# Optimization experiments

Hardware: AMD Instinct MI355X
Metric: run time of the kernel (lower is better)

## Reference

```python
import jax, jax.numpy as jnp
import numpy as np

HEADS = 16
D_MODEL = 1024
D_HEAD = D_MODEL // HEADS


def setup_inputs() -> dict:
    key = jax.random.key(0)
    ks = jax.random.split(key, 12)
    B, S = 4, 2048
    scale = D_MODEL ** -0.5
    inp = {
        "q": jax.random.normal(ks[0], (B, S, D_MODEL), jnp.float32),
        "k": jax.random.normal(ks[1], (B, S, D_MODEL), jnp.float32),
        "v": jax.random.normal(ks[2], (B, S, D_MODEL), jnp.float32),
        # causal mask: True = masked position
        "mask": jnp.triu(jnp.ones((S, S), bool), k=1)[None].repeat(B, axis=0),
        "wq": jax.random.normal(ks[3], (D_MODEL, D_MODEL), jnp.float32) * scale,
        "bq": jnp.zeros((D_MODEL,), jnp.float32),
        "wk": jax.random.normal(ks[4], (D_MODEL, D_MODEL), jnp.float32) * scale,
        "bk": jnp.zeros((D_MODEL,), jnp.float32),
        "wv": jax.random.normal(ks[5], (D_MODEL, D_MODEL), jnp.float32) * scale,
        "bv": jnp.zeros((D_MODEL,), jnp.float32),
        "wo": jax.random.normal(ks[6], (D_MODEL, D_MODEL), jnp.float32) * scale,
        "bo": jnp.zeros((D_MODEL,), jnp.float32),
    }
    return inp


def _split_head(x):
    B, S, _ = x.shape
    return x.reshape(B, S, HEADS, D_HEAD).transpose(0, 2, 1, 3)  # [B,H,S,D]


def reference(q, k, v, mask, wq, bq, wk, bk, wv, bv, wo, bo):
    # linear projections (torch Linear: x @ W^T + b)
    qh = _split_head(q @ wq.T + bq) * (D_HEAD ** -0.5)
    kh = _split_head(k @ wk.T + bk)
    vh = _split_head(v @ wv.T + bv)
    # scores [B,H,Sq,Sk]
    scores = jnp.einsum("bhqd,bhkd->bhqk", qh, kh)
    scores = jnp.where(mask[:, None, :, :], -1e20, scores)
    weights = jax.nn.softmax(scores, axis=-1)  # dropout p=0 in eval
    ctx = jnp.einsum("bhqk,bhkd->bhqd", weights, vh)
    B, H, S, D = ctx.shape
    ctx = ctx.transpose(0, 2, 1, 3).reshape(B, S, H * D)
    return ctx @ wo.T + bo
```

## Files before the change

### kernel.cpp

```cpp
#include <hip/hip_runtime.h>
#include <hip/hip_bf16.h>
#include <cstdint>
#include <cstddef>

typedef unsigned short u16;
typedef unsigned int u32;
using short8  = __attribute__((ext_vector_type(8))) short;
using f32x4   = __attribute__((ext_vector_type(4))) float;
using f32x16  = __attribute__((ext_vector_type(16))) float;
using u32x4   = __attribute__((ext_vector_type(4))) u32;

#define SCALE_Q 0.18033688011112043f

#define WAITVM(N) asm volatile("s_waitcnt vmcnt(" #N ")" ::: "memory")

__device__ inline u16 f2bf(float f) {
  return __builtin_bit_cast(u16, __float2bfloat16(f));
}

__device__ inline u32 cvt_pk_bf16(float a, float b) {
  u32 r;
  asm("v_cvt_pk_bf16_f32 %0, %1, %2" : "=v"(r) : "v"(a), "v"(b));
  return r;
}

__device__ inline f32x4 mfma16(short8 a, short8 b, f32x4 c) {
  return __builtin_amdgcn_mfma_f32_16x16x32_bf16(a, b, c, 0, 0, 0);
}
__device__ inline f32x16 mfma32(short8 a, short8 b, f32x16 c) {
  return __builtin_amdgcn_mfma_f32_32x32x16_bf16(a, b, c, 0, 0, 0);
}

__device__ inline void gload16(const void* g, void* l) {
  __builtin_amdgcn_global_load_lds(
      (const __attribute__((address_space(1))) void*)g,
      (__attribute__((address_space(3))) void*)l,
      16, 0, 0);
}

__global__ __launch_bounds__(256)
void prep(const float* __restrict__ q, const float* __restrict__ k,
          const float* __restrict__ v,
          const float* __restrict__ wq, const float* __restrict__ wk,
          const float* __restrict__ wv, const float* __restrict__ wo,
          u16* __restrict__ Wb, u16* __restrict__ Act) {
  const int c = blockIdx.x * 256 + threadIdx.x;
  const float* src;
  u16* dst;
  float sc = 1.f;
  size_t off;
  if (c < 524288) {
    const int m = c >> 17;
    off = (size_t)(c & 131071) * 8;
    src = (m == 0) ? wq : (m == 1) ? wk : (m == 2) ? wv : wo;
    if (m == 0) sc = SCALE_Q;
    dst = Wb + (size_t)m * 1048576;
  } else {
    const int c2 = c - 524288;
    const int m = c2 >> 20;
    off = (size_t)(c2 & 1048575) * 8;
    src = (m == 0) ? q : (m == 1) ? k : v;
    dst = Act + (size_t)m * 8388608;
  }
  f32x4 a = *(const f32x4*)(src + off);
  f32x4 b = *(const f32x4*)(src + off + 4);
  short8 vv;
#pragma unroll
  for (int j = 0; j < 4; ++j) { vv[j] = (short)f2bf(a[j] * sc); vv[4 + j] = (short)f2bf(b[j] * sc); }
  *(short8*)&dst[off] = vv;
}

struct GemmArgs {
  const u16* Act; const u16* ctx; const u16* Wb;
  const float* bq; const float* bk; const float* bv; const float* bo;
  u16* Qs; u16* Ks; u16* Vs; float* out;
};

__global__ __launch_bounds__(512)
void gemm_proj(GemmArgs ga, int modeBase) {
  const int mode = modeBase + blockIdx.z;
  const int bm = blockIdx.x, bn = blockIdx.y;
  const int tid = threadIdx.x;
  const int w = tid >> 6, lane = tid & 63;
  const int wr = w >> 1, wc = w & 1;
  const int l15 = lane & 15, g = lane >> 4;

  const u16* Am = (mode == 3) ? ga.ctx : ga.Act + (size_t)mode * 8388608;
  const u16* Wm = ga.Wb + (size_t)mode * 1048576;
  const float* bias = (mode == 0) ? ga.bq : (mode == 1) ? ga.bk : (mode == 2) ? ga.bv : ga.bo;

  __shared__ u16 As[4][256 * 32];
  __shared__ u16 Bs[4][128 * 32];

  f32x4 acc[4][4] = {};
  const int m0 = bm * 256, n0 = bn * 128;

  const int trow = tid >> 2;
  const int scol = (tid & 3) ^ ((tid >> 3) & 3);
  const int dstA0 = w * 512;
  const int dstA1 = 4096 + w * 512;
  const int dstB  = w * 512;

  auto stage = [&](int k0, int slot) {
    gload16(Am + (size_t)(m0 + trow) * 1024 + k0 + scol * 8,        &As[slot][dstA0]);
    gload16(Am + (size_t)(m0 + 128 + trow) * 1024 + k0 + scol * 8,  &As[slot][dstA1]);
    gload16(Wm + (size_t)(n0 + trow) * 1024 + k0 + scol * 8,        &Bs[slot][dstB]);
  };

  const int rsw = ((l15 >> 1) & 3);

  auto compute = [&](int slot) {
    short8 av[4], bv4[4];
#pragma unroll
    for (int mi = 0; mi < 4; ++mi)
      av[mi] = *(const short8*)&As[slot][(wr * 64 + mi * 16 + l15) * 32 + (g ^ rsw) * 8];
#pragma unroll
    for (int ni = 0; ni < 4; ++ni)
      bv4[ni] = *(const short8*)&Bs[slot][(wc * 64 + ni * 16 + l15) * 32 + (g ^ rsw) * 8];
#pragma unroll
    for (int mi = 0; mi < 4; ++mi)
#pragma unroll
      for (int ni = 0; ni < 4; ++ni)
        acc[mi][ni] = mfma16(av[mi], bv4[ni], acc[mi][ni]);
  };

  stage(0, 0);
  stage(32, 1);

  for (int tt = 0; tt < 28; tt += 4) {
#pragma unroll
    for (int u = 0; u < 4; ++u) {
      stage((tt + u + 2) * 32, (u + 2) & 3);
      __builtin_amdgcn_sched_barrier(0);
      WAITVM(6);
      __builtin_amdgcn_s_barrier();
      __builtin_amdgcn_sched_barrier(0);
      compute(u);
    }
  }
  stage(30 * 32, 2);
  __builtin_amdgcn_sched_barrier(0);
  WAITVM(6);
  __builtin_amdgcn_s_barrier();
  __builtin_amdgcn_sched_barrier(0);
  compute(0);

  stage(31 * 32, 3);
  __builtin_amdgcn_sched_barrier(0);
  WAITVM(6);
  __builtin_amdgcn_s_barrier();
  __builtin_amdgcn_sched_barrier(0);
  compute(1);

  WAITVM(3);
  __builtin_amdgcn_s_barrier();
  __builtin_amdgcn_sched_barrier(0);
  compute(2);

  WAITVM(0);
  __builtin_amdgcn_s_barrier();
  __builtin_amdgcn_sched_barrier(0);
  compute(3);

  float bvals[4];
#pragma unroll
  for (int ni = 0; ni < 4; ++ni)
    bvals[ni] = bias[n0 + wc * 64 + ni * 16 + l15] * ((mode == 0) ? SCALE_Q : 1.f);

  if (mode == 3) {
#pragma unroll
    for (int mi = 0; mi < 4; ++mi)
#pragma unroll
      for (int ni = 0; ni < 4; ++ni)
#pragma unroll
        for (int r = 0; r < 4; ++r) {
          const int m = m0 + wr * 64 + mi * 16 + g * 4 + r;
          const int n = n0 + wc * 64 + ni * 16 + l15;
          ga.out[(size_t)m * 1024 + n] = acc[mi][ni][r] + bvals[ni];
        }
  } else {
    u16* O = (mode == 0) ? ga.Qs : (mode == 1) ? ga.Ks : ga.Vs;
#pragma unroll
    for (int mi = 0; mi < 4; ++mi)
#pragma unroll
      for (int ni = 0; ni < 4; ++ni)
#pragma unroll
        for (int r = 0; r < 4; ++r) {
          const int m = m0 + wr * 64 + mi * 16 + g * 4 + r;
          const int n = n0 + wc * 64 + ni * 16 + l15;
          const int b = m >> 11, s = m & 2047, hh = n >> 6, d = n & 63;
          const float val = acc[mi][ni][r] + bvals[ni];
          const size_t base = (size_t)(b * 16 + hh) * 131072;
          size_t idx;
          if (mode == 2) {
            const int sp = (s & ~12) | ((s & 4) << 1) | ((s & 8) >> 1);
            const int kt = sp >> 5, w5 = sp & 31;
            const int j = ((d >> 5) << 1) | (w5 >> 4);
            const int hi2 = (w5 >> 3) & 1, e = w5 & 7;
            idx = base + (size_t)kt * 2048 + j * 512 + hi2 * 256 + (d & 31) * 8 + e;
          } else {
            const int s32 = s >> 5, l31 = s & 31;
            const int t2 = d >> 4, hi2 = (d >> 3) & 1, e = d & 7;
            idx = base + (size_t)s32 * 2048 + t2 * 512 + hi2 * 256 + l31 * 8 + e;
          }
          O[idx] = f2bf(val);
        }
  }
}

__global__ __launch_bounds__(256)
void attn_fwd(const u16* __restrict__ Qs, const u16* __restrict__ Ks,
              const u16* __restrict__ Vs, u16* __restrict__ ctx) {
  const int bh = blockIdx.x;
  const int qt = 15 - blockIdx.y;
  const int tid = threadIdx.x;
  const int w = tid >> 6, lane = tid & 63;
  const int l31 = lane & 31, hi = lane >> 5;

  const u16* Qb = Qs + (size_t)bh * 131072;
  const u16* Kb = Ks + (size_t)bh * 131072 + lane * 8;
  const u16* Vb = Vs + (size_t)bh * 131072 + lane * 8;
  const int b = bh >> 4, hh = bh & 15;

  const int qw0 = qt * 128 + w * 32;
  const int nkt = (qw0 >> 5) + 1;
  const int qrow = qw0 + l31;

  short8 qf[4];
  {
    const u16* qp = Qb + (size_t)(qw0 >> 5) * 2048 + lane * 8;
#pragma unroll
    for (int t = 0; t < 4; ++t) qf[t] = *(const short8*)(qp + t * 512);
  }

  f32x16 oacc0 = {}, oacc1 = {};
  float lsum = 0.f;

  auto body = [&](const short8* kf, const short8* vf, int kt, bool last) {
    f32x16 st = {};
    st = mfma32(kf[0], qf[0], st);
    st = mfma32(kf[1], qf[1], st);
    st = mfma32(kf[2], qf[2], st);
    st = mfma32(kf[3], qf[3], st);
    if (last) {
#pragma unroll
      for (int r = 0; r < 16; ++r) {
        const int ka = kt * 32 + (r & 3) + 8 * (r >> 2) + 4 * hi;
        if (ka > qrow) st[r] = -1e30f;
      }
    }
    float p[16];
#pragma unroll
    for (int r = 0; r < 16; ++r) p[r] = __builtin_amdgcn_exp2f(st[r]);
    {
      float s0 = (p[0] + p[1]) + (p[2] + p[3]);
      float s1 = (p[4] + p[5]) + (p[6] + p[7]);
      float s2 = (p[8] + p[9]) + (p[10] + p[11]);
      float s3 = (p[12] + p[13]) + (p[14] + p[15]);
      lsum += (s0 + s1) + (s2 + s3);
    }
    u32x4 a0, a1;
#pragma unroll
    for (int v2 = 0; v2 < 4; ++v2) {
      a0[v2] = cvt_pk_bf16(p[2 * v2], p[2 * v2 + 1]);
      a1[v2] = cvt_pk_bf16(p[8 + 2 * v2], p[9 + 2 * v2]);
    }
    const short8 pb0 = __builtin_bit_cast(short8, a0);
    const short8 pb1 = __builtin_bit_cast(short8, a1);
    oacc0 = mfma32(vf[0], pb0, oacc0);
    oacc0 = mfma32(vf[1], pb1, oacc0);
    oacc1 = mfma32(vf[2], pb0, oacc1);
    oacc1 = mfma32(vf[3], pb1, oacc1);
  };

  short8 kA[4], vA[4], kB[4], vB[4];
#pragma unroll
  for (int t = 0; t < 4; ++t) {
    kA[t] = *(const short8*)(Kb + t * 512);
    vA[t] = *(const short8*)(Vb + t * 512);
  }

  for (int kt = 0; ; ) {
    const bool lastA = (kt + 1 == nkt);
    if (!lastA) {
      const u16* kp = Kb + (size_t)(kt + 1) * 2048;
      const u16* vp = Vb + (size_t)(kt + 1) * 2048;
#pragma unroll
      for (int t = 0; t < 4; ++t) {
        kB[t] = *(const short8*)(kp + t * 512);
        vB[t] = *(const short8*)(vp + t * 512);
      }
    }
    body(kA, vA, kt, lastA);
    if (lastA) break;
    ++kt;
    const bool lastB = (kt + 1 == nkt);
    if (!lastB) {
      const u16* kp = Kb + (size_t)(kt + 1) * 2048;
      const u16* vp = Vb + (size_t)(kt + 1) * 2048;
#pragma unroll
      for (int t = 0; t < 4; ++t) {
        kA[t] = *(const short8*)(kp + t * 512);
        vA[t] = *(const short8*)(vp + t * 512);
      }
    }
    body(kB, vB, kt, lastB);
    if (lastB) break;
    ++kt;
  }

  lsum += __shfl_xor(lsum, 32);
  const float inv = __builtin_amdgcn_rcpf(lsum);

  u16* crow = ctx + ((size_t)(b * 2048 + qrow)) * 1024 + hh * 64;
#pragma unroll
  for (int r = 0; r < 16; r += 2) {
    const int d0 = (r & 3) + 8 * (r >> 2) + 4 * hi;
    *(u32*)&crow[d0]      = cvt_pk_bf16(oacc0[r] * inv, oacc0[r + 1] * inv);
    *(u32*)&crow[32 + d0] = cvt_pk_bf16(oacc1[r] * inv, oacc1[r + 1] * inv);
  }
}

extern "C" void kernel_launch(void* const* d_in, const int* in_sizes, int n_in,
                              void* d_out, int out_size, void* d_ws, size_t ws_size,
                              hipStream_t stream) {
  const float* q  = (const float*)d_in[0];
  const float* k  = (const float*)d_in[1];
  const float* v  = (const float*)d_in[2];
  const float* wq = (const float*)d_in[4];
  const float* bq = (const float*)d_in[5];
  const float* wk = (const float*)d_in[6];
  const float* bk = (const float*)d_in[7];
  const float* wv = (const float*)d_in[8];
  const float* bv = (const float*)d_in[9];
  const float* wo = (const float*)d_in[10];
  const float* bo = (const float*)d_in[11];

  char* ws = (char*)d_ws;
  const size_t WBSZ  = (size_t)4 * 1048576 * sizeof(u16);
  const size_t ACTSZ = (size_t)3 * 8388608 * sizeof(u16);
  const size_t SZ    = (size_t)64 * 131072 * sizeof(u16);
  u16* Wb  = (u16*)(ws);
  u16* Act = (u16*)(ws + WBSZ);
  u16* Qs  = (u16*)(ws + WBSZ + ACTSZ);
  u16* Ks  = (u16*)(ws + WBSZ + ACTSZ + SZ);
  u16* Vs  = (u16*)(ws + WBSZ + ACTSZ + 2 * SZ);
  u16* ctx = (u16*)(ws + WBSZ + ACTSZ + 3 * SZ);

  GemmArgs ga;
  ga.Act = Act; ga.ctx = ctx; ga.Wb = Wb;
  ga.bq = bq; ga.bk = bk; ga.bv = bv; ga.bo = bo;
  ga.Qs = Qs; ga.Ks = Ks; ga.Vs = Vs; ga.out = (float*)d_out;

  prep<<<dim3(14336), dim3(256), 0, stream>>>(q, k, v, wq, wk, wv, wo, Wb, Act);
  gemm_proj<<<dim3(32, 8, 3), dim3(512), 0, stream>>>(ga, 0);
  attn_fwd<<<dim3(64, 16), dim3(256), 0, stream>>>(Qs, Ks, Vs, ctx);
  gemm_proj<<<dim3(32, 8, 1), dim3(512), 0, stream>>>(ga, 3);
}
```

Measured before the change: 187.3 us.

## Rewrite projection GEMM with 256x256 tiles, BK=64 ping-pong pipeline and priority hints

The projection GEMM moves from 256x128 tiles with a 4-slot BK=32 pipeline to 256x256 tiles with BK=64 double-buffered LDS, XOR-swizzled staging, and 8 waves laid out 2x4. Each wave computes a 128x64 sub-tile in interleaved quarter steps, with LDS reads and global loads staged between barriers. The aim is more reuse per loaded byte and better overlap of loads with MFMA. s_setprio hints are also added around the MFMA groups in the GEMM and the attention kernel. The cost is higher register pressure (32 accumulators per lane), 128KB of LDS, and half as many blocks.

```diff
diff --git a/kernel.cpp b/kernel.cpp
--- a/kernel.cpp
+++ b/kernel.cpp
@@ -13,6 +13,9 @@
 #define SCALE_Q 0.18033688011112043f
 
 #define WAITVM(N) asm volatile("s_waitcnt vmcnt(" #N ")" ::: "memory")
+#define LGKM0 do { asm volatile("s_waitcnt lgkmcnt(0)" ::: "memory"); \
+                   __builtin_amdgcn_sched_barrier(0); } while (0)
+#define BARX __builtin_amdgcn_s_barrier()
 
 __device__ inline u16 f2bf(float f) {
   return __builtin_bit_cast(u16, __float2bfloat16(f));
@@ -76,91 +79,114 @@
   u16* Qs; u16* Ks; u16* Vs; float* out;
 };
 
-__global__ __launch_bounds__(512)
+__global__ __launch_bounds__(512, 2)
 void gemm_proj(GemmArgs ga, int modeBase) {
   const int mode = modeBase + blockIdx.z;
   const int bm = blockIdx.x, bn = blockIdx.y;
   const int tid = threadIdx.x;
-  const int w = tid >> 6, lane = tid & 63;
-  const int wr = w >> 1, wc = w & 1;
+  const int wid = tid >> 6, lane = tid & 63;
+  const int wr = wid >> 2, wc = wid & 3;
   const int l15 = lane & 15, g = lane >> 4;
+  const int r3 = l15 & 7;
 
   const u16* Am = (mode == 3) ? ga.ctx : ga.Act + (size_t)mode * 8388608;
   const u16* Wm = ga.Wb + (size_t)mode * 1048576;
   const float* bias = (mode == 0) ? ga.bq : (mode == 1) ? ga.bk : (mode == 2) ? ga.bv : ga.bo;
 
-  __shared__ u16 As[4][256 * 32];
-  __shared__ u16 Bs[4][128 * 32];
-
-  f32x4 acc[4][4] = {};
-  const int m0 = bm * 256, n0 = bn * 128;
-
-  const int trow = tid >> 2;
-  const int scol = (tid & 3) ^ ((tid >> 3) & 3);
-  const int dstA0 = w * 512;
-  const int dstA1 = 4096 + w * 512;
-  const int dstB  = w * 512;
-
-  auto stage = [&](int k0, int slot) {
-    gload16(Am + (size_t)(m0 + trow) * 1024 + k0 + scol * 8,        &As[slot][dstA0]);
-    gload16(Am + (size_t)(m0 + 128 + trow) * 1024 + k0 + scol * 8,  &As[slot][dstA1]);
-    gload16(Wm + (size_t)(n0 + trow) * 1024 + k0 + scol * 8,        &Bs[slot][dstB]);
-  };
-
-  const int rsw = ((l15 >> 1) & 3);
-
-  auto compute = [&](int slot) {
-    short8 av[4], bv4[4];
-#pragma unroll
-    for (int mi = 0; mi < 4; ++mi)
-      av[mi] = *(const short8*)&As[slot][(wr * 64 + mi * 16 + l15) * 32 + (g ^ rsw) * 8];
-#pragma unroll
-    for (int ni = 0; ni < 4; ++ni)
-      bv4[ni] = *(const short8*)&Bs[slot][(wc * 64 + ni * 16 + l15) * 32 + (g ^ rsw) * 8];
-#pragma unroll
-    for (int mi = 0; mi < 4; ++mi)
-#pragma unroll
-      for (int ni = 0; ni < 4; ++ni)
-        acc[mi][ni] = mfma16(av[mi], bv4[ni], acc[mi][ni]);
-  };
-
-  stage(0, 0);
-  stage(32, 1);
-
-  for (int tt = 0; tt < 28; tt += 4) {
-#pragma unroll
-    for (int u = 0; u < 4; ++u) {
-      stage((tt + u + 2) * 32, (u + 2) & 3);
-      __builtin_amdgcn_sched_barrier(0);
-      WAITVM(6);
-      __builtin_amdgcn_s_barrier();
-      __builtin_amdgcn_sched_barrier(0);
-      compute(u);
-    }
-  }
-  stage(30 * 32, 2);
-  __builtin_amdgcn_sched_barrier(0);
-  WAITVM(6);
-  __builtin_amdgcn_s_barrier();
-  __builtin_amdgcn_sched_barrier(0);
-  compute(0);
-
-  stage(31 * 32, 3);
-  __builtin_amdgcn_sched_barrier(0);
-  WAITVM(6);
-  __builtin_amdgcn_s_barrier();
-  __builtin_amdgcn_sched_barrier(0);
-  compute(1);
-
-  WAITVM(3);
-  __builtin_amdgcn_s_barrier();
-  __builtin_amdgcn_sched_barrier(0);
-  compute(2);
-
-  WAITVM(0);
-  __builtin_amdgcn_s_barrier();
-  __builtin_amdgcn_sched_barrier(0);
-  compute(3);
+  __shared__ u16 AS[2][2][128 * 64];
+  __shared__ u16 BS[2][2][128 * 64];
+
+  const int m0 = bm * 256, n0 = bn * 256;
+
+  f32x4 acc[8][4] = {};
+  short8 av[4][2], bvA[2][2], bvB[2][2];
+
+  auto stA = [&](int db, int half, int t) {
+    const u16* src = Am + (size_t)(m0 + half * 128) * 1024 + t * 64;
+    const int c0 = wid * 64 + lane, r0 = c0 >> 3;
+    gload16(src + (size_t)r0 * 1024 + (size_t)(((c0 & 7) ^ (r0 & 7)) * 8),
+            &AS[db][half][wid * 512]);
+    const int c1 = 512 + wid * 64 + lane, r1 = c1 >> 3;
+    gload16(src + (size_t)r1 * 1024 + (size_t)(((c1 & 7) ^ (r1 & 7)) * 8),
+            &AS[db][half][4096 + wid * 512]);
+  };
+  auto stB = [&](int db, int half, int t) {
+    const u16* src = Wm + (size_t)(n0 + half * 128) * 1024 + t * 64;
+    const int c0 = wid * 64 + lane, r0 = c0 >> 3;
+    gload16(src + (size_t)r0 * 1024 + (size_t)(((c0 & 7) ^ (r0 & 7)) * 8),
+            &BS[db][half][wid * 512]);
+    const int c1 = 512 + wid * 64 + lane, r1 = c1 >> 3;
+    gload16(src + (size_t)r1 * 1024 + (size_t)(((c1 & 7) ^ (r1 & 7)) * 8),
+            &BS[db][half][4096 + wid * 512]);
+  };
+
+  auto rdA = [&](int db, int mb) {
+    const u16* base = &AS[db][wr][0];
+#pragma unroll
+    for (int mi = 0; mi < 4; ++mi) {
+      const int row = (mb + mi) * 16 + l15;
+#pragma unroll
+      for (int kk = 0; kk < 2; ++kk)
+        av[mi][kk] = *(const short8*)&base[row * 64 + ((kk * 4 + g) ^ r3) * 8];
+    }
+  };
+  auto rdB = [&](int db, short8 (&bv)[2][2], int nb) {
+    const u16* base = &BS[db][wc >> 1][0];
+#pragma unroll
+    for (int ni = 0; ni < 2; ++ni) {
+      const int row = (wc & 1) * 64 + (nb + ni) * 16 + l15;
+#pragma unroll
+      for (int kk = 0; kk < 2; ++kk)
+        bv[ni][kk] = *(const short8*)&base[row * 64 + ((kk * 4 + g) ^ r3) * 8];
+    }
+  };
+  auto mm = [&](int mb, short8 (&bv)[2][2], int nb) {
+    __builtin_amdgcn_s_setprio(1);
+#pragma unroll
+    for (int kk = 0; kk < 2; ++kk)
+#pragma unroll
+      for (int mi = 0; mi < 4; ++mi)
+#pragma unroll
+        for (int ni = 0; ni < 2; ++ni)
+          acc[mb + mi][nb + ni] = mfma16(av[mi][kk], bv[ni][kk], acc[mb + mi][nb + ni]);
+    __builtin_amdgcn_s_setprio(0);
+  };
+
+  stA(0, 0, 0); stA(0, 1, 0); stB(0, 0, 0); stB(0, 1, 0);
+  stB(1, 0, 1); stB(1, 1, 1);
+  WAITVM(4);
+  BARX;
+
+  for (int i = 0; i < 8; ++i) {
+    const int t0 = 2 * i;
+    const bool lastIt = (i == 7);
+    rdA(0, 0); rdB(0, bvA, 0);
+    stA(1, 0, t0 + 1);
+    BARX; LGKM0; mm(0, bvA, 0); BARX;
+    rdB(0, bvB, 2);
+    stA(1, 1, t0 + 1);
+    BARX; LGKM0; mm(0, bvB, 2); BARX;
+    rdA(0, 4);
+    if (!lastIt) stB(0, 0, t0 + 2);
+    BARX; LGKM0; mm(4, bvB, 2); BARX;
+    if (!lastIt) stB(0, 1, t0 + 2);
+    BARX; mm(4, bvA, 0);
+    if (lastIt) { WAITVM(0); } else { WAITVM(4); }
+    BARX;
+    rdA(1, 0); rdB(1, bvA, 0);
+    if (!lastIt) stA(0, 0, t0 + 2);
+    BARX; LGKM0; mm(0, bvA, 0); BARX;
+    rdB(1, bvB, 2);
+    if (!lastIt) stA(0, 1, t0 + 2);
+    BARX; LGKM0; mm(0, bvB, 2); BARX;
+    rdA(1, 4);
+    if (!lastIt) stB(1, 0, t0 + 3);
+    BARX; LGKM0; mm(4, bvB, 2); BARX;
+    if (!lastIt) stB(1, 1, t0 + 3);
+    BARX; mm(4, bvA, 0);
+    if (!lastIt) { WAITVM(4); }
+    BARX;
+  }
 
   float bvals[4];
 #pragma unroll
@@ -169,24 +195,24 @@
 
   if (mode == 3) {
 #pragma unroll
-    for (int mi = 0; mi < 4; ++mi)
+    for (int mi = 0; mi < 8; ++mi)
 #pragma unroll
       for (int ni = 0; ni < 4; ++ni)
 #pragma unroll
         for (int r = 0; r < 4; ++r) {
-          const int m = m0 + wr * 64 + mi * 16 + g * 4 + r;
+          const int m = m0 + wr * 128 + mi * 16 + g * 4 + r;
           const int n = n0 + wc * 64 + ni * 16 + l15;
           ga.out[(size_t)m * 1024 + n] = acc[mi][ni][r] + bvals[ni];
         }
   } else {
     u16* O = (mode == 0) ? ga.Qs : (mode == 1) ? ga.Ks : ga.Vs;
 #pragma unroll
-    for (int mi = 0; mi < 4; ++mi)
+    for (int mi = 0; mi < 8; ++mi)
 #pragma unroll
       for (int ni = 0; ni < 4; ++ni)
 #pragma unroll
         for (int r = 0; r < 4; ++r) {
-          const int m = m0 + wr * 64 + mi * 16 + g * 4 + r;
+          const int m = m0 + wr * 128 + mi * 16 + g * 4 + r;
           const int n = n0 + wc * 64 + ni * 16 + l15;
           const int b = m >> 11, s = m & 2047, hh = n >> 6, d = n & 63;
           const float val = acc[mi][ni][r] + bvals[ni];
@@ -238,10 +264,12 @@
 
   auto body = [&](const short8* kf, const short8* vf, int kt, bool last) {
     f32x16 st = {};
+    __builtin_amdgcn_s_setprio(1);
     st = mfma32(kf[0], qf[0], st);
     st = mfma32(kf[1], qf[1], st);
     st = mfma32(kf[2], qf[2], st);
     st = mfma32(kf[3], qf[3], st);
+    __builtin_amdgcn_s_setprio(0);
     if (last) {
 #pragma unroll
       for (int r = 0; r < 16; ++r) {
@@ -267,10 +295,12 @@
     }
     const short8 pb0 = __builtin_bit_cast(short8, a0);
     const short8 pb1 = __builtin_bit_cast(short8, a1);
+    __builtin_amdgcn_s_setprio(1);
     oacc0 = mfma32(vf[0], pb0, oacc0);
     oacc0 = mfma32(vf[1], pb1, oacc0);
     oacc1 = mfma32(vf[2], pb0, oacc1);
     oacc1 = mfma32(vf[3], pb1, oacc1);
+    __builtin_amdgcn_s_setprio(0);
   };
 
   short8 kA[4], vA[4], kB[4], vB[4];
@@ -353,7 +383,7 @@
   ga.Qs = Qs; ga.Ks = Ks; ga.Vs = Vs; ga.out = (float*)d_out;
 
   prep<<<dim3(14336), dim3(256), 0, stream>>>(q, k, v, wq, wk, wv, wo, Wb, Act);
-  gemm_proj<<<dim3(32, 8, 3), dim3(512), 0, stream>>>(ga, 0);
+  gemm_proj<<<dim3(32, 4, 3), dim3(512), 0, stream>>>(ga, 0);
   attn_fwd<<<dim3(64, 16), dim3(256), 0, stream>>>(Qs, Ks, Vs, ctx);
-  gemm_proj<<<dim3(32, 8, 1), dim3(512), 0, stream>>>(ga, 3);
-}
+  gemm_proj<<<dim3(32, 4, 1), dim3(512), 0, stream>>>(ga, 3);
+}
```

After: 209.5 us. +11.9%, slower.
